# Performance work log

Measured on AMD Instinct MI355X. Metric: run time of the kernel, lower is better.

The kernel has to match this reference:

```python
import jax, jax.numpy as jnp
import numpy as np

B, L, D = 128, 196, 1024  # batch, att_size, rnn_size


def setup_inputs() -> dict:
    key = jax.random.key(0)
    ks = jax.random.split(key, 11)
    s = 1.0 / np.sqrt(D)
    return {
        "x": jax.random.normal(ks[0], (B, D), jnp.float32),
        "att": jax.random.normal(ks[1], (B, L, D), jnp.float32),
        "h": jax.random.normal(ks[2], (B, D), jnp.float32),
        "W_a2a": jax.random.uniform(ks[3], (D, D), jnp.float32, -s, s),
        "b_a2a": jax.random.uniform(ks[4], (D,), jnp.float32, -s, s),
        "W_h2a": jax.random.uniform(ks[5], (D, D), jnp.float32, -s, s),
        "b_h2a": jax.random.uniform(ks[6], (D,), jnp.float32, -s, s),
        "W_i2a": jax.random.uniform(ks[7], (D, D), jnp.float32, -s, s),
        "b_i2a": jax.random.uniform(ks[8], (D,), jnp.float32, -s, s),
        "W_d2d": jax.random.uniform(ks[9], (D,), jnp.float32, -s, s),
        "b_d2d": jax.random.uniform(ks[10], (), jnp.float32, -s, s),
    }


def reference(x, att, h, W_a2a, b_a2a, W_h2a, b_h2a, W_i2a, b_i2a, W_d2d, b_d2d):
    # att_v_1: [B, L, D]
    att_v = jnp.einsum('bld,ed->ble', att, W_a2a) + b_a2a
    att_h = (h @ W_h2a.T + b_h2a)[:, None, :]   # [B, 1, D]
    att_x = (x @ W_i2a.T + b_i2a)[:, None, :]   # [B, 1, D]
    dot = jnp.tanh(att_v + att_h + att_x)       # [B, L, D]
    scores = jnp.einsum('bld,d->bl', dot, W_d2d) + b_d2d  # [B, L]
    weight = jax.nn.softmax(scores, axis=-1)    # [B, L]
    att_res = jnp.einsum('bld,bl->bd', att, weight)  # [B, D]
    return att_res
```

## Files before the change

### kernel.cpp

```cpp
#include <hip/hip_runtime.h>
#include <hip/hip_bf16.h>

#define B_ 128
#define L_ 196
#define D_ 1024

typedef __attribute__((ext_vector_type(8))) short short8v;
typedef __attribute__((ext_vector_type(4))) float f32x4;
typedef unsigned short ushort_t;

#define OFF_ATTBF   0UL
#define OFF_WBF     51380224UL
#define OFF_A2      53477376UL
#define OFF_W2      54001664UL
#define OFF_C       58195968UL
#define OFF_SPART   58720256UL

__device__ inline unsigned short f2bf(float f) {
  unsigned int u = __float_as_uint(f);
  unsigned int r = (u + 0x7fffu + ((u >> 16) & 1u)) >> 16;
  return (unsigned short)r;
}

__global__ void convert_kernel(const float* __restrict__ att, const float* __restrict__ Wa,
                               const float* __restrict__ x,   const float* __restrict__ h,
                               const float* __restrict__ Wi,  const float* __restrict__ Wh,
                               ushort_t* __restrict__ att_bf, ushort_t* __restrict__ W_bf,
                               ushort_t* __restrict__ A2,     ushort_t* __restrict__ W2) {
  const int n0 = (B_*L_*D_)/4;
  const int n1 = (D_*D_)/4;
  const int n2 = (B_*D_)/4;
  const int total = n0 + n1 + 2*n2 + 2*n1;
  for (int idx = blockIdx.x*blockDim.x + threadIdx.x; idx < total;
       idx += gridDim.x*blockDim.x) {
    const float4* src; ushort_t* dst;
    int i = idx;
    if (i < n0)               { src = (const float4*)att + i; dst = att_bf + (size_t)i*4; }
    else if ((i -= n0) < n1)  { src = (const float4*)Wa  + i; dst = W_bf  + (size_t)i*4; }
    else if ((i -= n1) < n2)  { int b = i>>8, k4 = i&255; src = (const float4*)x  + i; dst = A2 + b*2048 + k4*4; }
    else if ((i -= n2) < n2)  { int b = i>>8, k4 = i&255; src = (const float4*)h  + i; dst = A2 + b*2048 + 1024 + k4*4; }
    else if ((i -= n2) < n1)  { int e = i>>8, k4 = i&255; src = (const float4*)Wi + i; dst = W2 + e*2048 + k4*4; }
    else { i -= n1;             int e = i>>8, k4 = i&255; src = (const float4*)Wh + i; dst = W2 + e*2048 + 1024 + k4*4; }
    float4 v = *src;
    ushort4 o; o.x = f2bf(v.x); o.y = f2bf(v.y); o.z = f2bf(v.z); o.w = f2bf(v.w);
    *(ushort4*)dst = o;
  }
}

__device__ inline void stage_tile(const ushort_t* __restrict__ g, int row0, int K, int k0,
                                  ushort_t* ldst, int t) {
  #pragma unroll
  for (int it = 0; it < 4; ++it) {
    int linear = it*4096 + t*16;
    int r = linear >> 7;
    int c = (t & 7) ^ (r & 7);
    const ushort_t* src = g + (size_t)(row0 + r)*K + k0 + c*8;
    ushort_t* dst = ldst + ((it*4096 + ((t & 192) << 4)) >> 1);
    __builtin_amdgcn_global_load_lds((const __attribute__((address_space(1))) void*)src,
                                     (__attribute__((address_space(3))) void*)dst,
                                     16, 0, 0);
  }
}

__device__ inline short8v ldfrag(const ushort_t* tile, int row, int c) {
  int phys = c ^ (row & 7);
  return *(const short8v*)(tile + row*64 + phys*8);
}

__global__ __launch_bounds__(256) void gemm_c_kernel(
    const ushort_t* __restrict__ Amat, const ushort_t* __restrict__ Bmat, int K,
    const float* __restrict__ ba, const float* __restrict__ bh, const float* __restrict__ bi,
    float* __restrict__ outc) {
  __shared__ ushort_t lds[32768];
  int bid = blockIdx.x;
  int m0 = 0, e0 = (bid & 7)*128;
  int t = threadIdx.x, lane = t & 63, w = t >> 6;
  int wm = w >> 1, we = w & 1;
  int lrow = lane & 15;
  int lk = lane >> 4;

  f32x4 acc[4][4];
  #pragma unroll
  for (int i = 0; i < 4; ++i)
    #pragma unroll
    for (int j = 0; j < 4; ++j) acc[i][j] = (f32x4){0.f, 0.f, 0.f, 0.f};

  stage_tile(Amat, m0, K, 0, lds, t);
  stage_tile(Bmat, e0, K, 0, lds + 8192, t);
  __syncthreads();

  int nk = K >> 6;
  for (int kt = 0; kt < nk; ++kt) {
    int cur = kt & 1;
    if (kt + 1 < nk) {
      stage_tile(Amat, m0, K, (kt+1) << 6, lds + (cur^1)*16384, t);
      stage_tile(Bmat, e0, K, (kt+1) << 6, lds + (cur^1)*16384 + 8192, t);
    }
    const ushort_t* At = lds + cur*16384;
    const ushort_t* Bt = At + 8192;
    #pragma unroll
    for (int hh = 0; hh < 2; ++hh) {
      short8v af[4], bfv[4];
      #pragma unroll
      for (int i = 0; i < 4; ++i) af[i]  = ldfrag(At, wm*64 + i*16 + lrow, hh*4 + lk);
      #pragma unroll
      for (int j = 0; j < 4; ++j) bfv[j] = ldfrag(Bt, we*64 + j*16 + lrow, hh*4 + lk);
      #pragma unroll
      for (int i = 0; i < 4; ++i)
        #pragma unroll
        for (int j = 0; j < 4; ++j)
          acc[i][j] = __builtin_amdgcn_mfma_f32_16x16x32_bf16(af[i], bfv[j], acc[i][j], 0, 0, 0);
    }
    __syncthreads();
  }

  #pragma unroll
  for (int i = 0; i < 4; ++i) {
    int m = m0 + wm*64 + i*16 + lk*4;
    #pragma unroll
    for (int j = 0; j < 4; ++j) {
      int e = e0 + we*64 + j*16 + lrow;
      float bsum = ba[e] + bh[e] + bi[e];
      #pragma unroll
      for (int r = 0; r < 4; ++r)
        outc[(m + r)*1024 + e] = acc[i][j][r] + bsum;
    }
  }
}

__device__ inline short8v ldfrag2(const ushort_t* tile, int row, int c) {
  int phys = c ^ (row & 7);
  return *(const short8v*)(tile + row*64 + phys*8);
}

__device__ inline void stage_half(const ushort_t* __restrict__ g, int row0, int Kdim,
                                  int kt, int half, ushort_t* lds_tile, int t, int w) {
  #pragma unroll
  for (int it2 = 0; it2 < 2; ++it2) {
    int linear = it2*8192 + t*16;
    int r = linear >> 7;
    int pc = (linear >> 4) & 7;
    int c = pc ^ (r & 7);
    const ushort_t* src = g + (size_t)(row0 + half*128 + r)*Kdim + kt*64 + c*8;
    ushort_t* dst = lds_tile + half*8192 + it2*4096 + w*512;
    __builtin_amdgcn_global_load_lds((const __attribute__((address_space(1))) void*)src,
                                     (__attribute__((address_space(3))) void*)dst,
                                     16, 0, 0);
  }
}

#define SB0()   __builtin_amdgcn_sched_barrier(0)
#define BARR()  __builtin_amdgcn_s_barrier()
#define LGKM0() asm volatile("s_waitcnt lgkmcnt(0)" ::: "memory")
#define VM6()   asm volatile("s_waitcnt vmcnt(6)" ::: "memory")

#define RD_A_LO(base) { _Pragma("unroll") for (int i_=0;i_<4;++i_) { int rr = wm*64 + i_*16 + lrow; \
    a[i_][0]=ldfrag2(base, rr, lk); a[i_][1]=ldfrag2(base, rr, 4+lk);} }
#define RD_A_HI(base) { _Pragma("unroll") for (int i_=0;i_<4;++i_) { int rr = 128 + wm*64 + i_*16 + lrow; \
    a[i_][0]=ldfrag2(base, rr, lk); a[i_][1]=ldfrag2(base, rr, 4+lk);} }
#define RD_B_LO(base) { _Pragma("unroll") for (int j_=0;j_<2;++j_) { int rr = wn*64 + j_*16 + lrow; \
    b[j_][0]=ldfrag2(base, rr, lk); b[j_][1]=ldfrag2(base, rr, 4+lk);} }
#define RD_B_HI(base) { _Pragma("unroll") for (int j_=0;j_<2;++j_) { int rr = wn*64 + (2+j_)*16 + lrow; \
    b[2+j_][0]=ldfrag2(base, rr, lk); b[2+j_][1]=ldfrag2(base, rr, 4+lk);} }

#define MFMAQ(I0, J0) { _Pragma("unroll") for (int i_=0;i_<4;++i_) { _Pragma("unroll") for (int j_=0;j_<2;++j_) { \
    acc[(I0)+i_][(J0)+j_] = __builtin_amdgcn_mfma_f32_16x16x32_bf16(a[i_][0], b[(J0)+j_][0], acc[(I0)+i_][(J0)+j_], 0,0,0); \
    acc[(I0)+i_][(J0)+j_] = __builtin_amdgcn_mfma_f32_16x16x32_bf16(a[i_][1], b[(J0)+j_][1], acc[(I0)+i_][(J0)+j_], 0,0,0); } } }

#define PH_TAIL(I0, J0) SB0(); BARR(); LGKM0(); SB0(); \
    __builtin_amdgcn_s_setprio(1); MFMAQ(I0, J0); __builtin_amdgcn_s_setprio(0); SB0(); BARR();

__global__ __launch_bounds__(512, 2) void gemm_score_kernel(
    const ushort_t* __restrict__ Amat, const ushort_t* __restrict__ Bmat,
    const float* __restrict__ cmat, const float* __restrict__ wd,
    float* __restrict__ spart) {
  __shared__ ushort_t lds[65536];
  const int K = 1024, nk = 16, NI = 8;
  int bid = blockIdx.x;
  int swz = (bid & 7)*49 + (bid >> 3);
  int m_blk = swz >> 2, e_blk = swz & 3;
  int m0 = m_blk*256, e0 = e_blk*256;
  int t = (int)threadIdx.x, lane = t & 63, w = t >> 6;
  int wm = w >> 2, wn = w & 3;
  int lrow = lane & 15, lk = lane >> 4;

  ushort_t* A0_ = lds;
  ushort_t* B0_ = lds + 16384;
  ushort_t* A1_ = lds + 32768;
  ushort_t* B1_ = lds + 49152;

  f32x4 acc[8][4];
  #pragma unroll
  for (int i = 0; i < 8; ++i)
    #pragma unroll
    for (int j = 0; j < 4; ++j) acc[i][j] = (f32x4){0.f, 0.f, 0.f, 0.f};
  short8v a[4][2], b[4][2];

  stage_half(Amat, m0, K, 0, 0, A0_, t, w);
  stage_half(Amat, m0, K, 0, 1, A0_, t, w);
  stage_half(Bmat, e0, K, 0, 0, B0_, t, w);
  stage_half(Bmat, e0, K, 0, 1, B0_, t, w);
  stage_half(Amat, m0, K, 1, 0, A1_, t, w);
  stage_half(Bmat, e0, K, 1, 0, B1_, t, w);
  stage_half(Bmat, e0, K, 1, 1, B1_, t, w);
  VM6(); SB0(); BARR();

  for (int itr = 0; itr < NI; ++itr) {
    int kt0 = 2*itr;
    int kc2 = (kt0+2 < nk) ? kt0+2 : nk-1;
    int kc3 = (kt0+3 < nk) ? kt0+3 : nk-1;
    RD_A_LO(A0_); RD_B_LO(B0_);
    stage_half(Amat, m0, K, kt0+1, 1, A1_, t, w);
    PH_TAIL(0,0);
    RD_B_HI(B0_);
    stage_half(Amat, m0, K, kc2, 0, A0_, t, w);
    PH_TAIL(0,2);
    RD_A_HI(A0_);
    stage_half(Bmat, e0, K, kc2, 0, B0_, t, w);
    PH_TAIL(4,0);
    stage_half(Bmat, e0, K, kc2, 1, B0_, t, w);
    VM6();
    PH_TAIL(4,2);
    RD_A_LO(A1_); RD_B_LO(B1_);
    stage_half(Amat, m0, K, kc2, 1, A0_, t, w);
    PH_TAIL(0,0);
    RD_B_HI(B1_);
    stage_half(Amat, m0, K, kc3, 0, A1_, t, w);
    PH_TAIL(0,2);
    RD_A_HI(A1_);
    stage_half(Bmat, e0, K, kc3, 0, B1_, t, w);
    PH_TAIL(4,0);
    stage_half(Bmat, e0, K, kc3, 1, B1_, t, w);
    VM6();
    PH_TAIL(4,2);
  }

  #pragma unroll
  for (int i = 0; i < 8; ++i) {
    int mbase = m0 + (i>>2)*128 + wm*64 + (i&3)*16 + lk*4;
    #pragma unroll
    for (int r = 0; r < 4; ++r) {
      int m = mbase + r;
      int bb = (int)((unsigned)m / 196u);
      float partial = 0.f;
      #pragma unroll
      for (int j = 0; j < 4; ++j) {
        int e = e0 + wn*64 + j*16 + lrow;
        float v = acc[i][j][r] + cmat[bb*1024 + e];
        float ex = __expf(2.f*v);
        partial += (1.f - 2.f/(ex + 1.f)) * wd[e];
      }
      partial += __shfl_xor(partial, 1);
      partial += __shfl_xor(partial, 2);
      partial += __shfl_xor(partial, 4);
      partial += __shfl_xor(partial, 8);
      if (lrow == 0) spart[(size_t)m*16 + e_blk*4 + wn] = partial;
    }
  }
}

__global__ __launch_bounds__(256) void finalize_kernel(const float* __restrict__ att,
                                                       const float* __restrict__ spart,
                                                       float* __restrict__ out) {
  int b  = blockIdx.x >> 1;
  int dh = blockIdx.x & 1;
  int t  = threadIdx.x;
  __shared__ float wls[L_];
  __shared__ float red[8];

  float s = -1e30f;
  if (t < L_) {
    const float* sp = spart + (size_t)(b*L_ + t)*16;
    float sum = 0.f;
    #pragma unroll
    for (int p = 0; p < 16; ++p) sum += sp[p];
    s = sum;
  }
  float m = s;
  #pragma unroll
  for (int off = 1; off < 64; off <<= 1) m = fmaxf(m, __shfl_xor(m, off));
  if ((t & 63) == 0) red[t >> 6] = m;
  __syncthreads();
  m = fmaxf(fmaxf(red[0], red[1]), fmaxf(red[2], red[3]));
  float p = (t < L_) ? __expf(s - m) : 0.f;
  float ssum = p;
  #pragma unroll
  for (int off = 1; off < 64; off <<= 1) ssum += __shfl_xor(ssum, off);
  if ((t & 63) == 0) red[4 + (t >> 6)] = ssum;
  __syncthreads();
  float tot = red[4] + red[5] + red[6] + red[7];
  if (t < L_) wls[t] = p / tot;
  __syncthreads();

  int d = dh*512 + t*2;
  const float* abase = att + (size_t)b*L_*D_ + d;
  float a0 = 0.f, a1 = 0.f;
  #pragma unroll 4
  for (int l = 0; l < L_; ++l) {
    float wv = wls[l];
    float2 av = *(const float2*)(abase + (size_t)l*D_);
    a0 += wv*av.x; a1 += wv*av.y;
  }
  float2 o; o.x = a0; o.y = a1;
  *(float2*)(out + (size_t)b*D_ + d) = o;
}

extern "C" void kernel_launch(void* const* d_in, const int* in_sizes, int n_in,
                              void* d_out, int out_size, void* d_ws, size_t ws_size,
                              hipStream_t stream) {
  (void)in_sizes; (void)n_in; (void)out_size; (void)ws_size;
  const float* x   = (const float*)d_in[0];
  const float* att = (const float*)d_in[1];
  const float* h   = (const float*)d_in[2];
  const float* Wa  = (const float*)d_in[3];
  const float* ba  = (const float*)d_in[4];
  const float* Wh  = (const float*)d_in[5];
  const float* bh  = (const float*)d_in[6];
  const float* Wi  = (const float*)d_in[7];
  const float* bi  = (const float*)d_in[8];
  const float* wd  = (const float*)d_in[9];

  char* ws = (char*)d_ws;
  ushort_t* att_bf = (ushort_t*)(ws + OFF_ATTBF);
  ushort_t* W_bf   = (ushort_t*)(ws + OFF_WBF);
  ushort_t* A2     = (ushort_t*)(ws + OFF_A2);
  ushort_t* W2     = (ushort_t*)(ws + OFF_W2);
  float*    cmat   = (float*)(ws + OFF_C);
  float*    spart  = (float*)(ws + OFF_SPART);
  float*    out    = (float*)d_out;

  hipLaunchKernelGGL(convert_kernel, dim3(2048), dim3(256), 0, stream,
                     att, Wa, x, h, Wi, Wh, att_bf, W_bf, A2, W2);
  hipLaunchKernelGGL(gemm_c_kernel, dim3(8), dim3(256), 0, stream,
                     A2, W2, 2048, ba, bh, bi, cmat);
  hipLaunchKernelGGL(gemm_score_kernel, dim3(392), dim3(512), 0, stream,
                     att_bf, W_bf, cmat, wd, spart);
  hipLaunchKernelGGL(finalize_kernel, dim3(256), dim3(256), 0, stream,
                     att, spart, out);
}
```

Before: 157.0 us.

## Split-K the bias GEMM, stage bias in LDS, and finalize from bf16 attention

The small x/h GEMM is split four ways along K, so it launches 32 blocks instead of 8 and writes partial sums. The score kernel adds those partials and all biases once into an LDS table, replacing per-element global reads of the bias matrix. Tile staging uses precomputed base pointers and drops the explicit scheduling barriers and LDS waits. Score partials are stored transposed as vector writes, and the finalize kernel reads the bf16 copy of att instead of fp32, halving its traffic at some cost in output precision.

```diff
diff --git a/kernel.cpp b/kernel.cpp
--- a/kernel.cpp
+++ b/kernel.cpp
@@ -13,8 +13,8 @@
 #define OFF_WBF     51380224UL
 #define OFF_A2      53477376UL
 #define OFF_W2      54001664UL
-#define OFF_C       58195968UL
-#define OFF_SPART   58720256UL
+#define OFF_SPART   53477376UL
+#define OFF_CPART   58195968UL
 
 __device__ inline unsigned short f2bf(float f) {
   unsigned int u = __float_as_uint(f);
@@ -47,14 +47,14 @@
   }
 }
 
-__device__ inline void stage_tile(const ushort_t* __restrict__ g, int row0, int K, int k0,
+__device__ inline void stage_tile(const ushort_t* __restrict__ g, int row0, int Kld, int k0,
                                   ushort_t* ldst, int t) {
   #pragma unroll
   for (int it = 0; it < 4; ++it) {
     int linear = it*4096 + t*16;
     int r = linear >> 7;
     int c = (t & 7) ^ (r & 7);
-    const ushort_t* src = g + (size_t)(row0 + r)*K + k0 + c*8;
+    const ushort_t* src = g + (size_t)(row0 + r)*Kld + k0 + c*8;
     ushort_t* dst = ldst + ((it*4096 + ((t & 192) << 4)) >> 1);
     __builtin_amdgcn_global_load_lds((const __attribute__((address_space(1))) void*)src,
                                      (__attribute__((address_space(3))) void*)dst,
@@ -68,12 +68,14 @@
 }
 
 __global__ __launch_bounds__(256) void gemm_c_kernel(
-    const ushort_t* __restrict__ Amat, const ushort_t* __restrict__ Bmat, int K,
-    const float* __restrict__ ba, const float* __restrict__ bh, const float* __restrict__ bi,
-    float* __restrict__ outc) {
+    const ushort_t* __restrict__ Amat, const ushort_t* __restrict__ Bmat,
+    float* __restrict__ cpart) {
   __shared__ ushort_t lds[32768];
   int bid = blockIdx.x;
-  int m0 = 0, e0 = (bid & 7)*128;
+  int e0 = (bid & 7)*128;
+  int kc = bid >> 3;
+  int kbeg = kc*512;
+  const int Kld = 2048;
   int t = threadIdx.x, lane = t & 63, w = t >> 6;
   int wm = w >> 1, we = w & 1;
   int lrow = lane & 15;
@@ -85,16 +87,16 @@
     #pragma unroll
     for (int j = 0; j < 4; ++j) acc[i][j] = (f32x4){0.f, 0.f, 0.f, 0.f};
 
-  stage_tile(Amat, m0, K, 0, lds, t);
-  stage_tile(Bmat, e0, K, 0, lds + 8192, t);
+  stage_tile(Amat, 0,  Kld, kbeg, lds, t);
+  stage_tile(Bmat, e0, Kld, kbeg, lds + 8192, t);
   __syncthreads();
 
-  int nk = K >> 6;
+  const int nk = 8;
   for (int kt = 0; kt < nk; ++kt) {
     int cur = kt & 1;
     if (kt + 1 < nk) {
-      stage_tile(Amat, m0, K, (kt+1) << 6, lds + (cur^1)*16384, t);
-      stage_tile(Bmat, e0, K, (kt+1) << 6, lds + (cur^1)*16384 + 8192, t);
+      stage_tile(Amat, 0,  Kld, kbeg + ((kt+1) << 6), lds + (cur^1)*16384, t);
+      stage_tile(Bmat, e0, Kld, kbeg + ((kt+1) << 6), lds + (cur^1)*16384 + 8192, t);
     }
     const ushort_t* At = lds + cur*16384;
     const ushort_t* Bt = At + 8192;
@@ -114,16 +116,16 @@
     __syncthreads();
   }
 
+  float* outc = cpart + (size_t)kc*131072;
   #pragma unroll
   for (int i = 0; i < 4; ++i) {
-    int m = m0 + wm*64 + i*16 + lk*4;
+    int m = wm*64 + i*16 + lk*4;
     #pragma unroll
     for (int j = 0; j < 4; ++j) {
       int e = e0 + we*64 + j*16 + lrow;
-      float bsum = ba[e] + bh[e] + bi[e];
       #pragma unroll
       for (int r = 0; r < 4; ++r)
-        outc[(m + r)*1024 + e] = acc[i][j][r] + bsum;
+        outc[(m + r)*1024 + e] = acc[i][j][r];
     }
   }
 }
@@ -133,25 +135,15 @@
   return *(const short8v*)(tile + row*64 + phys*8);
 }
 
-__device__ inline void stage_half(const ushort_t* __restrict__ g, int row0, int Kdim,
-                                  int kt, int half, ushort_t* lds_tile, int t, int w) {
-  #pragma unroll
-  for (int it2 = 0; it2 < 2; ++it2) {
-    int linear = it2*8192 + t*16;
-    int r = linear >> 7;
-    int pc = (linear >> 4) & 7;
-    int c = pc ^ (r & 7);
-    const ushort_t* src = g + (size_t)(row0 + half*128 + r)*Kdim + kt*64 + c*8;
-    ushort_t* dst = lds_tile + half*8192 + it2*4096 + w*512;
-    __builtin_amdgcn_global_load_lds((const __attribute__((address_space(1))) void*)src,
-                                     (__attribute__((address_space(3))) void*)dst,
-                                     16, 0, 0);
-  }
-}
-
-#define SB0()   __builtin_amdgcn_sched_barrier(0)
+#define STAGE(lanebase, half, kt, ldsT) { \
+    const ushort_t* s0_ = (lanebase) + (half)*131072 + (kt)*64; \
+    ushort_t* d0_ = (ldsT) + (half)*8192 + w*512; \
+    __builtin_amdgcn_global_load_lds((const __attribute__((address_space(1))) void*)s0_, \
+                                     (__attribute__((address_space(3))) void*)d0_, 16, 0, 0); \
+    __builtin_amdgcn_global_load_lds((const __attribute__((address_space(1))) void*)(s0_ + 65536), \
+                                     (__attribute__((address_space(3))) void*)(d0_ + 4096), 16, 0, 0); }
+
 #define BARR()  __builtin_amdgcn_s_barrier()
-#define LGKM0() asm volatile("s_waitcnt lgkmcnt(0)" ::: "memory")
 #define VM6()   asm volatile("s_waitcnt vmcnt(6)" ::: "memory")
 
 #define RD_A_LO(base) { _Pragma("unroll") for (int i_=0;i_<4;++i_) { int rr = wm*64 + i_*16 + lrow; \
@@ -163,19 +155,22 @@
 #define RD_B_HI(base) { _Pragma("unroll") for (int j_=0;j_<2;++j_) { int rr = wn*64 + (2+j_)*16 + lrow; \
     b[2+j_][0]=ldfrag2(base, rr, lk); b[2+j_][1]=ldfrag2(base, rr, 4+lk);} }
 
-#define MFMAQ(I0, J0) { _Pragma("unroll") for (int i_=0;i_<4;++i_) { _Pragma("unroll") for (int j_=0;j_<2;++j_) { \
-    acc[(I0)+i_][(J0)+j_] = __builtin_amdgcn_mfma_f32_16x16x32_bf16(a[i_][0], b[(J0)+j_][0], acc[(I0)+i_][(J0)+j_], 0,0,0); \
-    acc[(I0)+i_][(J0)+j_] = __builtin_amdgcn_mfma_f32_16x16x32_bf16(a[i_][1], b[(J0)+j_][1], acc[(I0)+i_][(J0)+j_], 0,0,0); } } }
-
-#define PH_TAIL(I0, J0) SB0(); BARR(); LGKM0(); SB0(); \
-    __builtin_amdgcn_s_setprio(1); MFMAQ(I0, J0); __builtin_amdgcn_s_setprio(0); SB0(); BARR();
+#define MFMAQ(I0, J0) { _Pragma("unroll") for (int k_=0;k_<2;++k_) { \
+    _Pragma("unroll") for (int i_=0;i_<4;++i_) { _Pragma("unroll") for (int j_=0;j_<2;++j_) { \
+      acc[(I0)+i_][(J0)+j_] = __builtin_amdgcn_mfma_f32_16x16x32_bf16(a[i_][k_], b[(J0)+j_][k_], acc[(I0)+i_][(J0)+j_], 0,0,0); } } } }
+
+#define PH_TAIL(I0, J0) BARR(); \
+    __builtin_amdgcn_s_setprio(1); MFMAQ(I0, J0); __builtin_amdgcn_s_setprio(0); BARR();
 
 __global__ __launch_bounds__(512, 2) void gemm_score_kernel(
     const ushort_t* __restrict__ Amat, const ushort_t* __restrict__ Bmat,
-    const float* __restrict__ cmat, const float* __restrict__ wd,
+    const float* __restrict__ cpart,
+    const float* __restrict__ ba, const float* __restrict__ bh, const float* __restrict__ bi,
+    const float* __restrict__ wd,
     float* __restrict__ spart) {
   __shared__ ushort_t lds[65536];
-  const int K = 1024, nk = 16, NI = 8;
+  __shared__ float c_lds[768];
+  const int nk = 16, NI = 8;
   int bid = blockIdx.x;
   int swz = (bid & 7)*49 + (bid >> 3);
   int m_blk = swz >> 2, e_blk = swz & 3;
@@ -184,6 +179,23 @@
   int wm = w >> 2, wn = w & 3;
   int lrow = lane & 15, lk = lane >> 4;
 
+  int bb0 = m0 / 196;
+  for (int idx = t; idx < 768; idx += 512) {
+    int bb = bb0 + (idx >> 8);
+    int e  = e0 + (idx & 255);
+    float v = ba[e] + bh[e] + bi[e];
+    if (bb < 128) {
+      v += cpart[bb*1024 + e] + cpart[131072 + bb*1024 + e]
+         + cpart[262144 + bb*1024 + e] + cpart[393216 + bb*1024 + e];
+    }
+    c_lds[idx] = v;
+  }
+
+  int r0 = t >> 3;
+  int c0 = (t & 7) ^ (r0 & 7);
+  const ushort_t* aBase = Amat + (size_t)(m0 + r0)*1024 + c0*8;
+  const ushort_t* bBase = Bmat + (size_t)(e0 + r0)*1024 + c0*8;
+
   ushort_t* A0_ = lds;
   ushort_t* B0_ = lds + 16384;
   ushort_t* A1_ = lds + 32768;
@@ -196,48 +208,50 @@
     for (int j = 0; j < 4; ++j) acc[i][j] = (f32x4){0.f, 0.f, 0.f, 0.f};
   short8v a[4][2], b[4][2];
 
-  stage_half(Amat, m0, K, 0, 0, A0_, t, w);
-  stage_half(Amat, m0, K, 0, 1, A0_, t, w);
-  stage_half(Bmat, e0, K, 0, 0, B0_, t, w);
-  stage_half(Bmat, e0, K, 0, 1, B0_, t, w);
-  stage_half(Amat, m0, K, 1, 0, A1_, t, w);
-  stage_half(Bmat, e0, K, 1, 0, B1_, t, w);
-  stage_half(Bmat, e0, K, 1, 1, B1_, t, w);
-  VM6(); SB0(); BARR();
+  STAGE(aBase, 0, 0, A0_);
+  STAGE(aBase, 1, 0, A0_);
+  STAGE(bBase, 0, 0, B0_);
+  STAGE(bBase, 1, 0, B0_);
+  STAGE(aBase, 0, 1, A1_);
+  STAGE(bBase, 0, 1, B1_);
+  STAGE(bBase, 1, 1, B1_);
+  VM6(); BARR();
 
   for (int itr = 0; itr < NI; ++itr) {
     int kt0 = 2*itr;
     int kc2 = (kt0+2 < nk) ? kt0+2 : nk-1;
     int kc3 = (kt0+3 < nk) ? kt0+3 : nk-1;
     RD_A_LO(A0_); RD_B_LO(B0_);
-    stage_half(Amat, m0, K, kt0+1, 1, A1_, t, w);
+    STAGE(aBase, 1, kt0+1, A1_);
     PH_TAIL(0,0);
     RD_B_HI(B0_);
-    stage_half(Amat, m0, K, kc2, 0, A0_, t, w);
+    STAGE(aBase, 0, kc2, A0_);
     PH_TAIL(0,2);
     RD_A_HI(A0_);
-    stage_half(Bmat, e0, K, kc2, 0, B0_, t, w);
+    STAGE(bBase, 0, kc2, B0_);
     PH_TAIL(4,0);
-    stage_half(Bmat, e0, K, kc2, 1, B0_, t, w);
+    STAGE(bBase, 1, kc2, B0_);
     VM6();
     PH_TAIL(4,2);
     RD_A_LO(A1_); RD_B_LO(B1_);
-    stage_half(Amat, m0, K, kc2, 1, A0_, t, w);
+    STAGE(aBase, 1, kc2, A0_);
     PH_TAIL(0,0);
     RD_B_HI(B1_);
-    stage_half(Amat, m0, K, kc3, 0, A1_, t, w);
+    STAGE(aBase, 0, kc3, A1_);
     PH_TAIL(0,2);
     RD_A_HI(A1_);
-    stage_half(Bmat, e0, K, kc3, 0, B1_, t, w);
+    STAGE(bBase, 0, kc3, B1_);
     PH_TAIL(4,0);
-    stage_half(Bmat, e0, K, kc3, 1, B1_, t, w);
+    STAGE(bBase, 1, kc3, B1_);
     VM6();
     PH_TAIL(4,2);
   }
 
+  int p = e_blk*4 + wn;
   #pragma unroll
   for (int i = 0; i < 8; ++i) {
     int mbase = m0 + (i>>2)*128 + wm*64 + (i&3)*16 + lk*4;
+    f32x4 ps;
     #pragma unroll
     for (int r = 0; r < 4; ++r) {
       int m = mbase + r;
@@ -245,21 +259,22 @@
       float partial = 0.f;
       #pragma unroll
       for (int j = 0; j < 4; ++j) {
-        int e = e0 + wn*64 + j*16 + lrow;
-        float v = acc[i][j][r] + cmat[bb*1024 + e];
+        int ee = wn*64 + j*16 + lrow;
+        float v = acc[i][j][r] + c_lds[(bb - bb0)*256 + ee];
         float ex = __expf(2.f*v);
-        partial += (1.f - 2.f/(ex + 1.f)) * wd[e];
+        partial += (1.f - 2.f/(ex + 1.f)) * wd[e0 + ee];
       }
       partial += __shfl_xor(partial, 1);
       partial += __shfl_xor(partial, 2);
       partial += __shfl_xor(partial, 4);
       partial += __shfl_xor(partial, 8);
-      if (lrow == 0) spart[(size_t)m*16 + e_blk*4 + wn] = partial;
-    }
-  }
-}
-
-__global__ __launch_bounds__(256) void finalize_kernel(const float* __restrict__ att,
+      ps[r] = partial;
+    }
+    if (lrow == 0) *(f32x4*)(spart + (size_t)p*25088 + mbase) = ps;
+  }
+}
+
+__global__ __launch_bounds__(256) void finalize_kernel(const ushort_t* __restrict__ att_bf,
                                                        const float* __restrict__ spart,
                                                        float* __restrict__ out) {
   int b  = blockIdx.x >> 1;
@@ -270,36 +285,38 @@
 
   float s = -1e30f;
   if (t < L_) {
-    const float* sp = spart + (size_t)(b*L_ + t)*16;
+    int m = b*L_ + t;
     float sum = 0.f;
     #pragma unroll
-    for (int p = 0; p < 16; ++p) sum += sp[p];
+    for (int p = 0; p < 16; ++p) sum += spart[p*25088 + m];
     s = sum;
   }
-  float m = s;
-  #pragma unroll
-  for (int off = 1; off < 64; off <<= 1) m = fmaxf(m, __shfl_xor(m, off));
-  if ((t & 63) == 0) red[t >> 6] = m;
+  float mx = s;
+  #pragma unroll
+  for (int off = 1; off < 64; off <<= 1) mx = fmaxf(mx, __shfl_xor(mx, off));
+  if ((t & 63) == 0) red[t >> 6] = mx;
   __syncthreads();
-  m = fmaxf(fmaxf(red[0], red[1]), fmaxf(red[2], red[3]));
-  float p = (t < L_) ? __expf(s - m) : 0.f;
-  float ssum = p;
+  mx = fmaxf(fmaxf(red[0], red[1]), fmaxf(red[2], red[3]));
+  float pr = (t < L_) ? __expf(s - mx) : 0.f;
+  float ssum = pr;
   #pragma unroll
   for (int off = 1; off < 64; off <<= 1) ssum += __shfl_xor(ssum, off);
   if ((t & 63) == 0) red[4 + (t >> 6)] = ssum;
   __syncthreads();
   float tot = red[4] + red[5] + red[6] + red[7];
-  if (t < L_) wls[t] = p / tot;
+  if (t < L_) wls[t] = pr / tot;
   __syncthreads();
 
   int d = dh*512 + t*2;
-  const float* abase = att + (size_t)b*L_*D_ + d;
+  const ushort_t* abase = att_bf + (size_t)b*L_*D_ + d;
   float a0 = 0.f, a1 = 0.f;
   #pragma unroll 4
   for (int l = 0; l < L_; ++l) {
     float wv = wls[l];
-    float2 av = *(const float2*)(abase + (size_t)l*D_);
-    a0 += wv*av.x; a1 += wv*av.y;
+    unsigned int v = *(const unsigned int*)(abase + (size_t)l*D_);
+    float lo = __uint_as_float(v << 16);
+    float hi = __uint_as_float(v & 0xffff0000u);
+    a0 += wv*lo; a1 += wv*hi;
   }
   float2 o; o.x = a0; o.y = a1;
   *(float2*)(out + (size_t)b*D_ + d) = o;
@@ -325,16 +342,16 @@
   ushort_t* W_bf   = (ushort_t*)(ws + OFF_WBF);
   ushort_t* A2     = (ushort_t*)(ws + OFF_A2);
   ushort_t* W2     = (ushort_t*)(ws + OFF_W2);
-  float*    cmat   = (float*)(ws + OFF_C);
+  float*    cpart  = (float*)(ws + OFF_CPART);
   float*    spart  = (float*)(ws + OFF_SPART);
   float*    out    = (float*)d_out;
 
   hipLaunchKernelGGL(convert_kernel, dim3(2048), dim3(256), 0, stream,
                      att, Wa, x, h, Wi, Wh, att_bf, W_bf, A2, W2);
-  hipLaunchKernelGGL(gemm_c_kernel, dim3(8), dim3(256), 0, stream,
-                     A2, W2, 2048, ba, bh, bi, cmat);
+  hipLaunchKernelGGL(gemm_c_kernel, dim3(32), dim3(256), 0, stream,
+                     A2, W2, cpart);
   hipLaunchKernelGGL(gemm_score_kernel, dim3(392), dim3(512), 0, stream,
-                     att_bf, W_bf, cmat, wd, spart);
+                     att_bf, W_bf, cpart, ba, bh, bi, wd, spart);
   hipLaunchKernelGGL(finalize_kernel, dim3(256), dim3(256), 0, stream,
-                     att, spart, out);
-}
+                     att_bf, spart, out);
+}
```

Result: faster. 129.5 us (-17.5%).
